# Performance work log

Hardware: AMD Instinct MI355X
Metric: run time of the kernel (lower is better)

Reference implementation:

```python
import jax, jax.numpy as jnp
import numpy as np

B, N = 8, 8192
S_ATTN, S_NONE = 128, 384          # npoint = (npoint_all=512, npoint_none_attn=384) -> npoint_attn=128
S = S_ATTN + S_NONE
NSAMPLE = 64
RADIUS = 0.4
D_FEAT = 64
MLP = [64, 64, 128]
IN_CH = 3 + D_FEAT


def fps(pts, K):
    # pytorch3d.sample_farthest_points, start index 0, full lengths. pts: [B,N,3]
    B_, N_, _ = pts.shape
    def body(carry, _):
        min_d2, last = carry
        lp = jnp.take_along_axis(pts, last[:, None, None], axis=1)      # [B,1,3]
        d2 = jnp.sum((pts - lp) ** 2, -1)                               # [B,N]
        min_d2 = jnp.minimum(min_d2, d2)
        nxt = jnp.argmax(min_d2, -1).astype(jnp.int32)
        return (min_d2, nxt), last
    init = (jnp.full((B_, N_), jnp.float32(1e10)), jnp.zeros((B_,), jnp.int32))
    _, idxs = jax.lax.scan(body, init, None, length=K)
    idxs = idxs.T                                                       # [B,K]
    sampled = jnp.take_along_axis(pts, idxs[..., None], axis=1)         # [B,K,3]
    return sampled, idxs


def ball_query(query, pts, K, radius):
    # pytorch3d.ball_query: first K points with d2 < r^2 in index order; idx pad=-1, nn pad=0.
    d2 = jnp.sum((query[:, :, None, :] - pts[:, None, :, :]) ** 2, -1)  # [B,S,N]
    mask = d2 < radius * radius
    order = jnp.cumsum(mask.astype(jnp.int32), -1) - 1
    slot = jnp.where(mask & (order < K), order, K)                      # overflow -> dump slot K
    n_ids = jnp.broadcast_to(jnp.arange(pts.shape[1], dtype=jnp.int32), slot.shape)
    def scatter_row(slot_row, ids_row):
        return jnp.full((K + 1,), -1, jnp.int32).at[slot_row].set(ids_row)[:K]
    idx = jax.vmap(jax.vmap(scatter_row))(slot, n_ids)                  # [B,S,K]
    valid = idx >= 0
    gathered = jax.vmap(lambda p, i: p[i])(pts, jnp.where(valid, idx, 0))  # [B,S,K,3]
    nn = jnp.where(valid[..., None], gathered, 0.0)
    return idx, nn


def _forward(xyz, points, attention, ws, bs):
    xyz_t = xyz.transpose(0, 2, 1)            # [B,N,3]
    pts_t = points.transpose(0, 2, 1)         # [B,N,D]
    attn_t = attention.transpose(0, 2, 1)     # [B,N,1]

    attn_xyz = attn_t * xyz_t
    none_xyz = (1.0 - attn_t) * xyz_t
    new_attn_xyz, idx_a = fps(attn_xyz, S_ATTN)
    new_none_xyz, idx_n = fps(none_xyz, S_NONE)
    new_xyz = jnp.concatenate([new_attn_xyz, new_none_xyz], axis=1)     # [B,S,3]
    fps_idx = jnp.concatenate([idx_a, idx_n], axis=1)                   # [B,S]
    new_attention = jnp.take_along_axis(attn_t, fps_idx[..., None], axis=1)  # [B,S,1]

    idx, grouped_xyz = ball_query(new_xyz, xyz_t, NSAMPLE, RADIUS)
    grouped_norm = grouped_xyz - new_xyz[:, :, None, :]                 # [B,S,K,3]
    gather_idx = jnp.where(idx < 0, N - 1, idx)   # torch index -1 wraps to last point
    grouped_pts = jax.vmap(lambda p, i: p[i])(pts_t, gather_idx)        # [B,S,K,D]
    feat = jnp.concatenate([grouped_norm, grouped_pts], -1)             # [B,S,K,3+D]

    x = feat.transpose(0, 3, 2, 1)                                      # [B,C,K,S]
    for w, b in zip(ws, bs):                                            # 1x1 Conv2d + ReLU
        x = jax.nn.relu(jnp.einsum('oc,bcks->boks', w, x) + b[None, :, None, None])
    new_points = jnp.max(x, axis=2)                                     # MaxPool over nsample -> [B,C',S]
    return new_xyz.transpose(0, 2, 1), new_points, new_attention.transpose(0, 2, 1)


def setup_inputs() -> dict:
    key = jax.random.key(0)
    ks = jax.random.split(key, 8)
    xyz = jax.random.normal(ks[0], (B, 3, N), jnp.float32)
    points = jax.random.normal(ks[1], (B, D_FEAT, N), jnp.float32)
    attention = jnp.round(jax.random.uniform(ks[2], (B, 1, N), jnp.float32))  # 0/1 mask
    inp = {'xyz': xyz, 'points': points, 'attention': attention}
    last = IN_CH
    for i, oc in enumerate(MLP):
        inp[f'w{i}'] = jax.random.normal(ks[3 + i], (oc, last), jnp.float32) / np.float32(np.sqrt(last))
        inp[f'b{i}'] = jnp.zeros((oc,), jnp.float32)
        last = oc
    return inp


def reference(xyz, points, attention, w0, b0, w1, b1, w2, b2):
    return _forward(xyz, points, attention, (w0, w1, w2), (b0, b1, b2))
```

## Files before the change

### kernel.cpp

```cpp
#include <hip/hip_runtime.h>
#include <cstdint>
#include <cstddef>

#define NB 8
#define NPTS 8192
#define S_TOT 512
#define NSAMP 64
#define DFEAT 64
#define INCH 67
#define SLOTS 17
#define CCAP (SLOTS * 256)
#define TDONE 1060
#define BALLW 13568

typedef __attribute__((ext_vector_type(8))) short v8s;
typedef __attribute__((ext_vector_type(4))) short v4s;
typedef __attribute__((ext_vector_type(4))) float v4f;

__device__ __forceinline__ float d2_exact(float ax, float ay, float az,
                                          float bx, float by, float bz) {
    float dx = __fsub_rn(ax, bx);
    float dy = __fsub_rn(ay, by);
    float dz = __fsub_rn(az, bz);
    return __fadd_rn(__fadd_rn(__fmul_rn(dx, dx), __fmul_rn(dy, dy)), __fmul_rn(dz, dz));
}

__device__ __forceinline__ unsigned short f2b(float f) {
    unsigned u = __float_as_uint(f);
    return (unsigned short)((u + 0x7fffu + ((u >> 16) & 1u)) >> 16);
}

__device__ __forceinline__ void st_wt_f32(float* p, float v) {
    __hip_atomic_store(p, v, __ATOMIC_RELAXED, __HIP_MEMORY_SCOPE_AGENT);
}
__device__ __forceinline__ void st_wt_u32(unsigned* p, unsigned v) {
    __hip_atomic_store(p, v, __ATOMIC_RELAXED, __HIP_MEMORY_SCOPE_AGENT);
}

template <int CTRL>
__device__ __forceinline__ unsigned long long dpp_max_u64(unsigned long long k) {
    int lo = (int)(unsigned)(k & 0xffffffffull);
    int hi = (int)(unsigned)(k >> 32);
    int slo = __builtin_amdgcn_update_dpp(lo, lo, CTRL, 0xf, 0xf, false);
    int shi = __builtin_amdgcn_update_dpp(hi, hi, CTRL, 0xf, 0xf, false);
    unsigned long long o = ((unsigned long long)(unsigned)shi << 32) | (unsigned)slo;
    return (o > k) ? o : k;
}

__device__ __forceinline__ void ball_one(
    const float* __restrict__ xyz,
    const unsigned short* __restrict__ ptsTh,
    const unsigned short* __restrict__ wp,
    const float* __restrict__ b0, const float* __restrict__ b1,
    const float* __restrict__ b2,
    const float* __restrict__ out0, float* __restrict__ out1,
    int b, int sg, int lane, short* sBuf, int* s_idx)
{
    const float R2 = (float)(0.4 * 0.4);
    int col = lane & 15, quad = lane >> 4, kq = quad * 8;

    const float* xb = xyz + (size_t)b * 3 * NPTS;
    float qx = out0[(size_t)b * 3 * S_TOT + sg];
    float qy = out0[(size_t)b * 3 * S_TOT + S_TOT + sg];
    float qz = out0[(size_t)b * 3 * S_TOT + 2 * S_TOT + sg];

    unsigned long long* s_mask = (unsigned long long*)sBuf;

#pragma unroll 8
    for (int j = 0; j < 128; j++) {
        int n = j * 64 + lane;
        float d2 = d2_exact(qx, qy, qz, xb[n], xb[NPTS + n], xb[2 * NPTS + n]);
        unsigned long long m = __ballot(d2 < R2);
        if (lane == 0) s_mask[j] = m;
    }

    unsigned long long m0 = s_mask[lane];
    unsigned long long m1 = s_mask[64 + lane];
    int c0 = (int)__popcll(m0), c1 = (int)__popcll(m1);
    int i0 = c0;
#pragma unroll
    for (int off = 1; off <= 32; off <<= 1) {
        int t = __shfl_up(i0, off);
        if (lane >= off) i0 += t;
    }
    int T0 = __shfl(i0, 63);
    int i1 = c1;
#pragma unroll
    for (int off = 1; off <= 32; off <<= 1) {
        int t = __shfl_up(i1, off);
        if (lane >= off) i1 += t;
    }
    int total = T0 + __shfl(i1, 63);
    int p0 = i0 - c0;
    int p1 = T0 + i1 - c1;

    {
        int base = p0, org = lane * 64;
        while (m0 && base < NSAMP) {
            int bp = __ffsll((long long)m0) - 1;
            s_idx[base++] = org + bp;
            m0 &= m0 - 1;
        }
        base = p1; org = (64 + lane) * 64;
        while (m1 && base < NSAMP) {
            int bp = __ffsll((long long)m1) - 1;
            s_idx[base++] = org + bp;
            m1 &= m1 - 1;
        }
    }
    int cnt = (total > NSAMP) ? NSAMP : total;

    int nb = (lane < cnt) ? s_idx[lane] : -1;
    float nx_ = 0.f, ny_ = 0.f, nz_ = 0.f;
    if (nb >= 0) { nx_ = xb[nb]; ny_ = xb[NPTS + nb]; nz_ = xb[2 * NPTS + nb]; }
    float fx = nx_ - qx, fy = ny_ - qy, fz = nz_ - qz;
    int row = (nb < 0) ? (NPTS - 1) : nb;

    {
        const unsigned short* ph = ptsTh + ((size_t)b * NPTS + row) * DFEAT;
        short* xr = &sBuf[lane * 104];
#pragma unroll
        for (int i = 0; i < 8; i++)
            *(v8s*)(xr + i * 8) = *(const v8s*)(ph + i * 8);
#pragma unroll
        for (int i = 0; i < 5; i++)
            *(v8s*)(xr + 64 + i * 8) = (v8s)0;
        v4s xyzp;
        xyzp[0] = (short)f2b(fx); xyzp[1] = (short)f2b(fy);
        xyzp[2] = (short)f2b(fz); xyzp[3] = 0;
        *(v4s*)(xr + 64) = xyzp;
    }

    const v8s* wpv = (const v8s*)wp;

    v4f acc[4][4];
#pragma unroll
    for (int nt = 0; nt < 4; nt++) {
        float bb = b0[nt * 16 + col];
#pragma unroll
        for (int mt = 0; mt < 4; mt++) acc[mt][nt] = (v4f){bb, bb, bb, bb};
    }
#pragma unroll
    for (int kt = 0; kt < 3; kt++) {
        v8s bf[4];
#pragma unroll
        for (int nt = 0; nt < 4; nt++) bf[nt] = wpv[(kt * 4 + nt) * 64 + lane];
#pragma unroll
        for (int mt = 0; mt < 4; mt++) {
            v8s a = *(const v8s*)&sBuf[(mt * 16 + col) * 104 + kt * 32 + kq];
#pragma unroll
            for (int nt = 0; nt < 4; nt++)
                acc[mt][nt] = __builtin_amdgcn_mfma_f32_16x16x32_bf16(a, bf[nt], acc[mt][nt], 0, 0, 0);
        }
    }
#pragma unroll
    for (int mt = 0; mt < 4; mt++)
#pragma unroll
        for (int nt = 0; nt < 4; nt++)
#pragma unroll
            for (int r = 0; r < 4; r++)
                sBuf[(mt * 16 + quad * 4 + r) * 72 + nt * 16 + col] =
                    (short)f2b(fmaxf(acc[mt][nt][r], 0.0f));

#pragma unroll
    for (int nt = 0; nt < 4; nt++) {
        float bb = b1[nt * 16 + col];
#pragma unroll
        for (int mt = 0; mt < 4; mt++) acc[mt][nt] = (v4f){bb, bb, bb, bb};
    }
#pragma unroll
    for (int kt = 0; kt < 2; kt++) {
        v8s bf[4];
#pragma unroll
        for (int nt = 0; nt < 4; nt++) bf[nt] = wpv[(12 + kt * 4 + nt) * 64 + lane];
#pragma unroll
        for (int mt = 0; mt < 4; mt++) {
            v8s a = *(const v8s*)&sBuf[(mt * 16 + col) * 72 + kt * 32 + kq];
#pragma unroll
            for (int nt = 0; nt < 4; nt++)
                acc[mt][nt] = __builtin_amdgcn_mfma_f32_16x16x32_bf16(a, bf[nt], acc[mt][nt], 0, 0, 0);
        }
    }
#pragma unroll
    for (int mt = 0; mt < 4; mt++)
#pragma unroll
        for (int nt = 0; nt < 4; nt++)
#pragma unroll
            for (int r = 0; r < 4; r++)
                sBuf[(mt * 16 + quad * 4 + r) * 72 + nt * 16 + col] =
                    (short)f2b(fmaxf(acc[mt][nt][r], 0.0f));

#pragma unroll
    for (int p = 0; p < 2; p++) {
#pragma unroll
        for (int nt = 0; nt < 4; nt++) {
            float bb = b2[(p * 4 + nt) * 16 + col];
#pragma unroll
            for (int mt = 0; mt < 4; mt++) acc[mt][nt] = (v4f){bb, bb, bb, bb};
        }
#pragma unroll
        for (int kt = 0; kt < 2; kt++) {
            v8s bf[4];
#pragma unroll
            for (int nt = 0; nt < 4; nt++)
                bf[nt] = wpv[(20 + kt * 8 + p * 4 + nt) * 64 + lane];
#pragma unroll
            for (int mt = 0; mt < 4; mt++) {
                v8s a = *(const v8s*)&sBuf[(mt * 16 + col) * 72 + kt * 32 + kq];
#pragma unroll
                for (int nt = 0; nt < 4; nt++)
                    acc[mt][nt] = __builtin_amdgcn_mfma_f32_16x16x32_bf16(a, bf[nt], acc[mt][nt], 0, 0, 0);
            }
        }
#pragma unroll
        for (int nt = 0; nt < 4; nt++) {
            float v = 0.0f;
#pragma unroll
            for (int mt = 0; mt < 4; mt++)
#pragma unroll
                for (int r = 0; r < 4; r++)
                    v = fmaxf(v, acc[mt][nt][r]);
            v = fmaxf(v, __shfl_xor(v, 16));
            v = fmaxf(v, __shfl_xor(v, 32));
            if (lane < 16)
                out1[((size_t)(b * 128 + (p * 4 + nt) * 16 + lane)) * S_TOT + sg] = v;
        }
    }
}

__global__ __launch_bounds__(256, 1) void fps_fused(
    const float* __restrict__ attn,
    int* __restrict__ hdr,
    float* __restrict__ out0, float* __restrict__ out2,
    const float* __restrict__ pts, unsigned short* __restrict__ ptsTh,
    const float* __restrict__ w0, const float* __restrict__ w1,
    const float* __restrict__ w2, unsigned short* __restrict__ wp,
    const float* __restrict__ xyz,
    const float* __restrict__ b0v, const float* __restrict__ b1v,
    const float* __restrict__ b2v,
    float* __restrict__ out1,
    int* __restrict__ prog, int* __restrict__ tcount, int* __restrict__ skip)
{
    __shared__ __align__(16) char smem[69632 + 6144 + 64];
    int blk = blockIdx.x;
    int tid = threadIdx.x;

    if (blk < 16) {
        int b = blk >> 1, grp = blk & 1;
        int K = grp ? 384 : 128;
        int soff = grp ? 128 : 0;
        int lane = tid & 63, wid = tid >> 6;
        const float* xb = xyz + (size_t)b * 3 * NPTS;
        const float* ab = attn + (size_t)b * NPTS;

        float4* sc = (float4*)smem;
        float4* s_obuf = (float4*)(smem + 69632);
        unsigned long long* s_red = (unsigned long long*)(smem + 69632 + 6144);
        int* s_init = (int*)(smem + 69632 + 6144);

        if (tid == 0) s_init[0] = NPTS;
        __syncthreads();

        int n0 = tid * 32;
        unsigned km = 0;
        int cnt = 0;
#pragma unroll
        for (int c = 0; c < 8; c++) {
            float4 a4 = *(const float4*)(ab + n0 + c * 4);
            const float* af = (const float*)&a4;
#pragma unroll
            for (int j = 0; j < 4; j++) {
                bool kp = grp ? (af[j] == 0.0f) : (af[j] != 0.0f);
                if (kp) { km |= 1u << (c * 4 + j); cnt++; }
            }
        }
        if (km != 0xFFFFFFFFu)
            atomicMin(&s_init[0], n0 + __builtin_ctz(~km));

        int incl = cnt;
#pragma unroll
        for (int off = 1; off <= 32; off <<= 1) {
            int t = __shfl_up(incl, off);
            if (lane >= off) incl += t;
        }
        if (lane == 63) s_init[1 + wid] = incl;
        __syncthreads();
        int woff = 0, tot = 0;
#pragma unroll
        for (int w = 0; w < 4; w++) {
            int v = s_init[1 + w];
            if (w < wid) woff += v;
            tot += v;
        }
        int rm = s_init[0];
        int M = tot + ((rm < NPTS) ? 1 : 0);
        int repslot = (rm < NPTS) ? rm : -1;
        if (tid == 0) { hdr[blk * 2] = M; hdr[blk * 2 + 1] = repslot; }
        if (M > CCAP) {
            if (tid == 0)
                __hip_atomic_store(&prog[blk], -1, __ATOMIC_RELAXED, __HIP_MEMORY_SCOPE_AGENT);
            return;
        }
        int pos = woff + incl - cnt;
        int rm_eff = (rm < NPTS) ? rm : 0x7fffffff;
#pragma unroll
        for (int c = 0; c < 8; c++) {
            if ((km >> (c * 4)) & 0xFu) {
                float4 xx = *(const float4*)(xb + n0 + c * 4);
                float4 yy = *(const float4*)(xb + NPTS + n0 + c * 4);
                float4 zz = *(const float4*)(xb + 2 * NPTS + n0 + c * 4);
                const float* xf = (const float*)&xx;
                const float* yf = (const float*)&yy;
                const float* zf = (const float*)&zz;
#pragma unroll
                for (int j = 0; j < 4; j++) {
                    if ((km >> (c * 4 + j)) & 1u) {
                        int idx = n0 + c * 4 + j;
                        int fin = pos + ((idx > rm_eff) ? 1 : 0);
                        sc[fin] = make_float4(xf[j], yf[j], zf[j], 0.0f);
                        pos++;
                    }
                }
            }
        }
        if (tid == 0 && rm < NPTS)
            sc[rm] = make_float4(__fmul_rn(0.0f, xb[rm]),
                                 __fmul_rn(0.0f, xb[NPTS + rm]),
                                 __fmul_rn(0.0f, xb[2 * NPTS + rm]), 0.0f);
        __syncthreads();
        __builtin_amdgcn_s_setprio(1);

        float px[SLOTS], py[SLOTS], pz[SLOTS], md[SLOTS];
#pragma unroll
        for (int i = 0; i < SLOTS; i++) {
            int sl = i * 256 + tid;
            bool v = sl < M;
            float4 c = sc[sl];
            px[i] = v ? c.x : 0.0f;
            py[i] = v ? c.y : 0.0f;
            pz[i] = v ? c.z : 0.0f;
            md[i] = v ? 1e10f : -1.0f;
        }
        float4 c0 = sc[0];
        float lx = c0.x, ly = c0.y, lz = c0.z;
        float a_last = ab[0];
        float kept_a = grp ? 0.0f : 1.0f;
        float rep_a  = grp ? 1.0f : 0.0f;

        for (int k = 0; k < K; k++) {
            if (tid == 0) s_obuf[k] = make_float4(lx, ly, lz, a_last);
            if (k == K - 1) break;

            float bv = -1.0f; int bslot = 0x7fffffff;
#pragma unroll
            for (int i = 0; i < SLOTS; i++) {
                float d2 = d2_exact(px[i], py[i], pz[i], lx, ly, lz);
                md[i] = fminf(md[i], d2);
                int sl = i * 256 + tid;
                bool w = (md[i] > bv) || ((md[i] == bv) && (sl < bslot));
                bv = w ? md[i] : bv;
                bslot = w ? sl : bslot;
            }
            unsigned long long key = (bv >= 0.0f)
                ? (((unsigned long long)__float_as_uint(bv) << 32) | (unsigned)(~bslot))
                : 0ull;
            key = dpp_max_u64<0x111>(key);
            key = dpp_max_u64<0x112>(key);
            key = dpp_max_u64<0x114>(key);
            key = dpp_max_u64<0x118>(key);
            key = dpp_max_u64<0x142>(key);
            key = dpp_max_u64<0x143>(key);
            int buf = k & 1;
            if (lane == 63) s_red[buf * 4 + wid] = key;
            __syncthreads();

            const unsigned long long* rp = &s_red[buf * 4];
            unsigned long long k0 = rp[0], k1 = rp[1], k2 = rp[2], k3 = rp[3];
            unsigned long long m01 = (k0 > k1) ? k0 : k1;
            unsigned long long m23 = (k2 > k3) ? k2 : k3;
            unsigned long long g = (m01 > m23) ? m01 : m23;
            int wslot = (int)(~(unsigned)g);
            float4 wc = sc[wslot];
            lx = wc.x; ly = wc.y; lz = wc.z;
            a_last = (wslot == repslot) ? rep_a : kept_a;

            if (((k & 15) == 15) && wid == 3) {
                asm volatile("s_waitcnt vmcnt(0)" ::: "memory");
                if (lane == 0 && k >= 31)
                    __hip_atomic_store(&prog[blk], k - 15, __ATOMIC_RELAXED, __HIP_MEMORY_SCOPE_AGENT);
                if (lane < 16) {
                    int kk = k - 15 + lane;
                    float4 o = s_obuf[kk];
                    int sgO = soff + kk;
                    size_t base = (size_t)b * 3 * S_TOT;
                    st_wt_f32(&out0[base + sgO], o.x);
                    st_wt_f32(&out0[base + S_TOT + sgO], o.y);
                    st_wt_f32(&out0[base + 2 * S_TOT + sgO], o.z);
                    st_wt_f32(&out2[(size_t)b * S_TOT + sgO], o.w);
                }
            }
        }
        __syncthreads();
        if (wid == 3) {
            if (lane < 16) {
                int kk = K - 16 + lane;
                float4 o = s_obuf[kk];
                int sgO = soff + kk;
                size_t base = (size_t)b * 3 * S_TOT;
                st_wt_f32(&out0[base + sgO], o.x);
                st_wt_f32(&out0[base + S_TOT + sgO], o.y);
                st_wt_f32(&out0[base + 2 * S_TOT + sgO], o.z);
                st_wt_f32(&out2[(size_t)b * S_TOT + sgO], o.w);
            }
            asm volatile("s_waitcnt vmcnt(0)" ::: "memory");
            if (lane == 0)
                __hip_atomic_store(&prog[blk], K, __ATOMIC_RELAXED, __HIP_MEMORY_SCOPE_AGENT);
        }
    } else if (blk < 16 + 1024) {
        float (*t)[65] = (float(*)[65])smem;
        int blk2 = blk - 16;
        int b = blk2 >> 7;
        int n0 = (blk2 & 127) * 64;
        int tx = tid & 63, ty = tid >> 6;
        for (int c = ty; c < 64; c += 4)
            t[c][tx] = pts[((size_t)b * DFEAT + c) * NPTS + n0 + tx];
        __syncthreads();
        {
            unsigned* pTu = (unsigned*)ptsTh;
            int txc = tid & 31, rr = tid >> 5;
            for (int r = rr; r < 64; r += 8) {
                unsigned lo = f2b(t[2 * txc][r]);
                unsigned hi = f2b(t[2 * txc + 1][r]);
                st_wt_u32(&pTu[((size_t)b * NPTS + n0 + r) * 32 + txc],
                          lo | (hi << 16));
            }
        }
        asm volatile("s_waitcnt vmcnt(0)" ::: "memory");
        __syncthreads();
        if (tid == 0)
            __hip_atomic_fetch_add(tcount, 1, __ATOMIC_RELAXED, __HIP_MEMORY_SCOPE_AGENT);
    } else if (blk < 1076) {
        if (tid < 64) {
            int t = blk - (16 + 1024), l = tid;
            int kq = (l >> 4) * 8, n16 = l & 15;
            unsigned short o[8];
#pragma unroll
            for (int j = 0; j < 8; j++) {
                float v;
                if (t < 12) {
                    int kt = t >> 2, nt = t & 3;
                    int k = kt * 32 + kq + j, n = nt * 16 + n16;
                    v = (k < 64) ? w0[n * INCH + 3 + k] : (k < 67 ? w0[n * INCH + (k - 64)] : 0.0f);
                } else if (t < 20) {
                    int tt = t - 12, kt = tt >> 2, nt = tt & 3;
                    v = w1[(nt * 16 + n16) * 64 + kt * 32 + kq + j];
                } else {
                    int tt = t - 20, kt = tt >> 3, nt = tt & 7;
                    v = w2[(nt * 16 + n16) * 64 + kt * 32 + kq + j];
                }
                o[j] = f2b(v);
            }
            unsigned* wpu = (unsigned*)wp;
            size_t baseu = (size_t)t * 256 + l * 4;
#pragma unroll
            for (int j = 0; j < 4; j++)
                st_wt_u32(&wpu[baseu + j],
                          (unsigned)o[2 * j] | ((unsigned)o[2 * j + 1] << 16));
            asm volatile("s_waitcnt vmcnt(0)" ::: "memory");
            if (tid == 0)
                __hip_atomic_fetch_add(tcount, 1, __ATOMIC_RELAXED, __HIP_MEMORY_SCOPE_AGENT);
        }
    } else {
        int lane = tid & 63, wid = tid >> 6;
        int w = (blk - 1076) * 4 + wid;
        int b, grp, kk;
        if (w < 2048) { kk = w >> 4; int r = w & 15; b = r & 7; grp = r >> 3; }
        else          { int w2 = w - 2048; kk = 128 + (w2 >> 3); b = w2 & 7; grp = 1; }
        int sg = (grp ? 128 : 0) + kk;
        int q = b * 512 + sg;
        int pblk = b * 2 + grp;

        int ok = 1;
        for (int to = 0;;) {
            int p = __hip_atomic_load(&prog[pblk], __ATOMIC_RELAXED, __HIP_MEMORY_SCOPE_AGENT);
            if (p < 0) { ok = 0; break; }
            if (p > kk) {
                int t = __hip_atomic_load(tcount, __ATOMIC_RELAXED, __HIP_MEMORY_SCOPE_AGENT);
                if (t >= TDONE) break;
            }
            if (++to > 500) { ok = 0; break; }
            __builtin_amdgcn_s_sleep(64);
        }
        if (!ok) {
            if (lane == 0) skip[q] = 1;
            return;
        }
        __builtin_amdgcn_fence(__ATOMIC_ACQUIRE, "agent");

        short* sBufW = (short*)(smem + wid * BALLW);
        int* s_idxW = (int*)(smem + wid * BALLW + 13312);
        ball_one(xyz, ptsTh, wp, b0v, b1v, b2v, out0, out1, b, sg, lane, sBufW, s_idxW);
    }
}

__global__ __launch_bounds__(1024, 1) void fps_kernel(
    const float* __restrict__ xyz, const float* __restrict__ attn,
    const int* __restrict__ hdr,
    float* __restrict__ out0, float* __restrict__ out2)
{
    int blk = blockIdx.x;
    if (hdr != nullptr && hdr[blk * 2] <= CCAP) return;
    int b = blk >> 1, grp = blk & 1;
    int K = grp ? 384 : 128;
    int soff = grp ? 128 : 0;
    int tid = threadIdx.x, lane = tid & 63, wid = tid >> 6;
    const float* xb = xyz + (size_t)b * 3 * NPTS;
    const float* ab = attn + (size_t)b * NPTS;

    float px[8], py[8], pz[8], md[8];
#pragma unroll
    for (int i = 0; i < 8; i++) {
        int n = tid + i * 1024;
        float a = ab[n];
        float f = grp ? __fsub_rn(1.0f, a) : a;
        px[i] = __fmul_rn(f, xb[n]);
        py[i] = __fmul_rn(f, xb[NPTS + n]);
        pz[i] = __fmul_rn(f, xb[2 * NPTS + n]);
        md[i] = 1e10f;
    }
    __shared__ unsigned long long s_red[2][16];
    float a_last = ab[0];
    float f0 = grp ? __fsub_rn(1.0f, a_last) : a_last;
    float lx = __fmul_rn(f0, xb[0]);
    float ly = __fmul_rn(f0, xb[NPTS]);
    float lz = __fmul_rn(f0, xb[2 * NPTS]);

    for (int k = 0; k < K; k++) {
        if (tid == 0) {
            int sg = soff + k;
            out0[(size_t)b * 3 * S_TOT + sg] = lx;
            out0[(size_t)b * 3 * S_TOT + S_TOT + sg] = ly;
            out0[(size_t)b * 3 * S_TOT + 2 * S_TOT + sg] = lz;
            out2[(size_t)b * S_TOT + sg] = a_last;
        }
        if (k == K - 1) break;
        float bv = -1.0f; int bi = 0;
#pragma unroll
        for (int i = 0; i < 8; i++) {
            float d2 = d2_exact(px[i], py[i], pz[i], lx, ly, lz);
            md[i] = fminf(md[i], d2);
            if (md[i] > bv) { bv = md[i]; bi = tid + i * 1024; }
        }
        unsigned long long best =
            ((unsigned long long)__float_as_uint(bv) << 32) | (unsigned)(~bi);
#pragma unroll
        for (int off = 32; off >= 1; off >>= 1) {
            unsigned long long o = __shfl_down(best, off);
            best = (o > best) ? o : best;
        }
        if (lane == 0) s_red[k & 1][wid] = best;
        __syncthreads();
        unsigned long long r = (lane < 16) ? s_red[k & 1][lane] : 0ull;
#pragma unroll
        for (int off = 8; off >= 1; off >>= 1) {
            unsigned long long o = __shfl_down(r, off);
            r = (o > r) ? o : r;
        }
        r = __shfl(r, 0);
        int n = (int)(~(unsigned)r);
        a_last = ab[n];
        float fl = grp ? __fsub_rn(1.0f, a_last) : a_last;
        lx = __fmul_rn(fl, xb[n]);
        ly = __fmul_rn(fl, xb[NPTS + n]);
        lz = __fmul_rn(fl, xb[2 * NPTS + n]);
    }
}

__global__ __launch_bounds__(256) void ball_tail(
    const float* __restrict__ xyz,
    const unsigned short* __restrict__ ptsTh,
    const unsigned short* __restrict__ wp,
    const float* __restrict__ b0, const float* __restrict__ b1,
    const float* __restrict__ b2,
    const float* __restrict__ out0, float* __restrict__ out1,
    const int* __restrict__ skip)
{
    __shared__ __align__(16) char smem[4 * BALLW];
    int lane = threadIdx.x & 63, wid = threadIdx.x >> 6;
    int q = blockIdx.x * 4 + wid;
    if (skip[q] == 0) return;
    int b = q >> 9, sg = q & 511;
    short* sBufW = (short*)(smem + wid * BALLW);
    int* s_idxW = (int*)(smem + wid * BALLW + 13312);
    ball_one(xyz, ptsTh, wp, b0, b1, b2, out0, out1, b, sg, lane, sBufW, s_idxW);
}

__global__ __launch_bounds__(64, 1) void ball_mlp_fb(
    const float* __restrict__ xyz, const float* __restrict__ pts,
    const float* __restrict__ w0, const float* __restrict__ b0,
    const float* __restrict__ w1, const float* __restrict__ b1,
    const float* __restrict__ w2, const float* __restrict__ b2,
    const float* __restrict__ out0, float* __restrict__ out1)
{
    const float R2 = (float)(0.4 * 0.4);
    int q = blockIdx.x;
    int b = q >> 9, sg = q & 511, lane = threadIdx.x;
    const float* xb = xyz + (size_t)b * 3 * NPTS;
    float qx = out0[(size_t)b * 3 * S_TOT + sg];
    float qy = out0[(size_t)b * 3 * S_TOT + S_TOT + sg];
    float qz = out0[(size_t)b * 3 * S_TOT + 2 * S_TOT + sg];

    __shared__ int s_idx[NSAMP];
    __shared__ float s_h[32 * 64];
    int cnt = 0;
    for (int base = 0; base < NPTS; base += 64) {
        int n = base + lane;
        float d2 = d2_exact(qx, qy, qz, xb[n], xb[NPTS + n], xb[2 * NPTS + n]);
        bool flag = d2 < R2;
        unsigned long long m = __ballot(flag);
        int pos = cnt + (int)__popcll(m & ((1ull << lane) - 1ull));
        if (flag && pos < NSAMP) s_idx[pos] = n;
        cnt += (int)__popcll(m);
    }
    if (cnt > NSAMP) cnt = NSAMP;
    int nb = (lane < cnt) ? s_idx[lane] : -1;
    float nx_ = 0.f, ny_ = 0.f, nz_ = 0.f;
    if (nb >= 0) { nx_ = xb[nb]; ny_ = xb[NPTS + nb]; nz_ = xb[2 * NPTS + nb]; }
    float fx = nx_ - qx, fy = ny_ - qy, fz = nz_ - qz;
    int row = (nb < 0) ? (NPTS - 1) : nb;

    float h1[64];
#pragma unroll
    for (int o = 0; o < 64; o++) {
        float a = __builtin_fmaf(w0[o * INCH + 0], fx, b0[o]);
        a = __builtin_fmaf(w0[o * INCH + 1], fy, a);
        h1[o] = __builtin_fmaf(w0[o * INCH + 2], fz, a);
    }
    const float* pb = pts + (size_t)b * DFEAT * NPTS + row;
#pragma unroll 1
    for (int c = 0; c < 64; c++) {
        float f = pb[(size_t)c * NPTS];
#pragma unroll
        for (int o = 0; o < 64; o++)
            h1[o] = __builtin_fmaf(w0[o * INCH + 3 + c], f, h1[o]);
    }
#pragma unroll
    for (int c = 0; c < 32; c++) s_h[c * 64 + lane] = fmaxf(h1[c], 0.0f);
    float h1h[32];
#pragma unroll
    for (int c = 0; c < 32; c++) h1h[c] = fmaxf(h1[32 + c], 0.0f);

    float h2[64];
#pragma unroll
    for (int o = 0; o < 64; o++) h2[o] = b1[o];
#pragma unroll 1
    for (int c = 0; c < 32; c++) {
        float hc = s_h[c * 64 + lane];
#pragma unroll
        for (int o = 0; o < 64; o++)
            h2[o] = __builtin_fmaf(w1[o * 64 + c], hc, h2[o]);
    }
#pragma unroll
    for (int c = 0; c < 32; c++) s_h[c * 64 + lane] = h1h[c];
#pragma unroll 1
    for (int c = 0; c < 32; c++) {
        float hc = s_h[c * 64 + lane];
#pragma unroll
        for (int o = 0; o < 64; o++)
            h2[o] = __builtin_fmaf(w1[o * 64 + (32 + c)], hc, h2[o]);
    }
#pragma unroll
    for (int o = 0; o < 64; o++) h2[o] = fmaxf(h2[o], 0.0f);

#pragma unroll 2
    for (int o = 0; o < 128; o++) {
        const float* wr = w2 + o * 64;
        float acc = b2[o];
#pragma unroll
        for (int c = 0; c < 64; c++) acc = __builtin_fmaf(wr[c], h2[c], acc);
        acc = fmaxf(acc, 0.0f);
#pragma unroll
        for (int off = 32; off >= 1; off >>= 1)
            acc = fmaxf(acc, __shfl_down(acc, off));
        if (lane == 0) out1[((size_t)(b * 128 + o)) * S_TOT + sg] = acc;
    }
}

extern "C" void kernel_launch(void* const* d_in, const int* in_sizes, int n_in,
                              void* d_out, int out_size, void* d_ws, size_t ws_size,
                              hipStream_t stream) {
    const float* xyz  = (const float*)d_in[0];
    const float* pts  = (const float*)d_in[1];
    const float* attn = (const float*)d_in[2];
    const float* w0 = (const float*)d_in[3];
    const float* b0 = (const float*)d_in[4];
    const float* w1 = (const float*)d_in[5];
    const float* b1 = (const float*)d_in[6];
    const float* w2 = (const float*)d_in[7];
    const float* b2 = (const float*)d_in[8];

    float* out0 = (float*)d_out;
    float* out1 = out0 + (size_t)NB * 3 * S_TOT;
    float* out2 = out1 + (size_t)NB * 128 * S_TOT;

    unsigned short* wp    = (unsigned short*)d_ws;
    unsigned short* ptsTh = (unsigned short*)((char*)d_ws + 36864);
    char*           cxyz  = (char*)d_ws + 36864 + 8388608;
    int*            hdr   = (int*)(cxyz + (size_t)16 * CCAP * 16);
    int*            prog  = hdr + 32;
    int*            tcnt  = prog + 16;
    int*            skip  = tcnt + 4;
    const size_t need = 36864 + 8388608 + (size_t)16 * CCAP * 16 + 128
                        + (16 + 4 + 4096) * 4 + 64;

    if (ws_size >= need) {
        hipMemsetAsync(prog, 0, (size_t)(16 + 4 + 4096) * 4, stream);
        fps_fused<<<16 + 1024 + 36 + 1024, 256, 0, stream>>>(
            attn, hdr, out0, out2, pts, ptsTh, w0, w1, w2, wp,
            xyz, b0, b1, b2, out1, prog, tcnt, skip);
        fps_kernel<<<16, 1024, 0, stream>>>(xyz, attn, hdr, out0, out2);
        ball_tail<<<1024, 256, 0, stream>>>(xyz, ptsTh, wp, b0, b1, b2,
                                            out0, out1, skip);
    } else {
        fps_kernel<<<16, 1024, 0, stream>>>(xyz, attn, nullptr, out0, out2);
        ball_mlp_fb<<<NB * S_TOT, 64, 0, stream>>>(xyz, pts, w0, b0, w1, b1,
                                                   w2, b2, out0, out1);
    }
}
```

Measured before the change: 611.5 us.

## Split FPS compaction into producer blocks and merge fallback and tail into one cleanup kernel

Point compaction moves out of the 16 FPS blocks into 16 separate producer blocks. These write the compacted coordinates to global workspace and raise a flag, and the FPS blocks spin on that flag before loading into registers and shared memory. The FPS inner-loop barrier becomes a raw s_waitcnt plus s_barrier, and an extra progress value is published earlier. The separate fps_kernel and ball_tail launches are replaced by one cleanup kernel that reruns FPS only for blocks that failed or overflowed, then handles the skipped ball queries once a counter is set. This cuts one launch and shortens the FPS critical path, but it adds cross-block spin-waits with timeouts that assume producer blocks get scheduled alongside the waiting blocks.

```diff
diff --git a/kernel.cpp b/kernel.cpp
--- a/kernel.cpp
+++ b/kernel.cpp
@@ -12,6 +12,7 @@
 #define CCAP (SLOTS * 256)
 #define TDONE 1060
 #define BALLW 13568
+#define SMEMSZ 82048
 
 typedef __attribute__((ext_vector_type(8))) short v8s;
 typedef __attribute__((ext_vector_type(4))) short v4s;
@@ -230,6 +231,7 @@
 
 __global__ __launch_bounds__(256, 1) void fps_fused(
     const float* __restrict__ attn,
+    float4* __restrict__ cxyz,
     int* __restrict__ hdr,
     float* __restrict__ out0, float* __restrict__ out2,
     const float* __restrict__ pts, unsigned short* __restrict__ ptsTh,
@@ -239,9 +241,10 @@
     const float* __restrict__ b0v, const float* __restrict__ b1v,
     const float* __restrict__ b2v,
     float* __restrict__ out1,
-    int* __restrict__ prog, int* __restrict__ tcount, int* __restrict__ skip)
+    int* __restrict__ prog, int* __restrict__ tcount, int* __restrict__ skip,
+    int* __restrict__ cflag, int* __restrict__ fpsdone)
 {
-    __shared__ __align__(16) char smem[69632 + 6144 + 64];
+    __shared__ __align__(16) char smem[SMEMSZ];
     int blk = blockIdx.x;
     int tid = threadIdx.x;
 
@@ -250,102 +253,49 @@
         int K = grp ? 384 : 128;
         int soff = grp ? 128 : 0;
         int lane = tid & 63, wid = tid >> 6;
-        const float* xb = xyz + (size_t)b * 3 * NPTS;
-        const float* ab = attn + (size_t)b * NPTS;
-
-        float4* sc = (float4*)smem;
-        float4* s_obuf = (float4*)(smem + 69632);
-        unsigned long long* s_red = (unsigned long long*)(smem + 69632 + 6144);
-        int* s_init = (int*)(smem + 69632 + 6144);
-
-        if (tid == 0) s_init[0] = NPTS;
-        __syncthreads();
-
-        int n0 = tid * 32;
-        unsigned km = 0;
-        int cnt = 0;
-#pragma unroll
-        for (int c = 0; c < 8; c++) {
-            float4 a4 = *(const float4*)(ab + n0 + c * 4);
-            const float* af = (const float*)&a4;
-#pragma unroll
-            for (int j = 0; j < 4; j++) {
-                bool kp = grp ? (af[j] == 0.0f) : (af[j] != 0.0f);
-                if (kp) { km |= 1u << (c * 4 + j); cnt++; }
-            }
-        }
-        if (km != 0xFFFFFFFFu)
-            atomicMin(&s_init[0], n0 + __builtin_ctz(~km));
-
-        int incl = cnt;
-#pragma unroll
-        for (int off = 1; off <= 32; off <<= 1) {
-            int t = __shfl_up(incl, off);
-            if (lane >= off) incl += t;
-        }
-        if (lane == 63) s_init[1 + wid] = incl;
-        __syncthreads();
-        int woff = 0, tot = 0;
-#pragma unroll
-        for (int w = 0; w < 4; w++) {
-            int v = s_init[1 + w];
-            if (w < wid) woff += v;
-            tot += v;
-        }
-        int rm = s_init[0];
-        int M = tot + ((rm < NPTS) ? 1 : 0);
-        int repslot = (rm < NPTS) ? rm : -1;
-        if (tid == 0) { hdr[blk * 2] = M; hdr[blk * 2 + 1] = repslot; }
+
+        int cok = 0;
+        for (int to = 0; to < 4000; ++to) {
+            if (__hip_atomic_load(&cflag[blk], __ATOMIC_RELAXED, __HIP_MEMORY_SCOPE_AGENT)) { cok = 1; break; }
+            __builtin_amdgcn_s_sleep(32);
+        }
+        if (!cok) {
+            if (tid == 0)
+                __hip_atomic_store(&prog[blk], -1, __ATOMIC_RELAXED, __HIP_MEMORY_SCOPE_AGENT);
+            return;
+        }
+        __builtin_amdgcn_fence(__ATOMIC_ACQUIRE, "agent");
+
+        int M = hdr[blk * 2];
+        int repslot = hdr[blk * 2 + 1];
         if (M > CCAP) {
             if (tid == 0)
                 __hip_atomic_store(&prog[blk], -1, __ATOMIC_RELAXED, __HIP_MEMORY_SCOPE_AGENT);
             return;
         }
-        int pos = woff + incl - cnt;
-        int rm_eff = (rm < NPTS) ? rm : 0x7fffffff;
-#pragma unroll
-        for (int c = 0; c < 8; c++) {
-            if ((km >> (c * 4)) & 0xFu) {
-                float4 xx = *(const float4*)(xb + n0 + c * 4);
-                float4 yy = *(const float4*)(xb + NPTS + n0 + c * 4);
-                float4 zz = *(const float4*)(xb + 2 * NPTS + n0 + c * 4);
-                const float* xf = (const float*)&xx;
-                const float* yf = (const float*)&yy;
-                const float* zf = (const float*)&zz;
-#pragma unroll
-                for (int j = 0; j < 4; j++) {
-                    if ((km >> (c * 4 + j)) & 1u) {
-                        int idx = n0 + c * 4 + j;
-                        int fin = pos + ((idx > rm_eff) ? 1 : 0);
-                        sc[fin] = make_float4(xf[j], yf[j], zf[j], 0.0f);
-                        pos++;
-                    }
-                }
-            }
-        }
-        if (tid == 0 && rm < NPTS)
-            sc[rm] = make_float4(__fmul_rn(0.0f, xb[rm]),
-                                 __fmul_rn(0.0f, xb[NPTS + rm]),
-                                 __fmul_rn(0.0f, xb[2 * NPTS + rm]), 0.0f);
-        __syncthreads();
         __builtin_amdgcn_s_setprio(1);
+
+        const float4* cb = cxyz + (size_t)blk * CCAP;
+        float4* sc = (float4*)smem;
+        float4* s_obuf = (float4*)(smem + 69632);
+        unsigned long long* s_red = (unsigned long long*)(smem + 69632 + 6144);
 
         float px[SLOTS], py[SLOTS], pz[SLOTS], md[SLOTS];
 #pragma unroll
         for (int i = 0; i < SLOTS; i++) {
             int sl = i * 256 + tid;
             bool v = sl < M;
-            float4 c = sc[sl];
-            px[i] = v ? c.x : 0.0f;
-            py[i] = v ? c.y : 0.0f;
-            pz[i] = v ? c.z : 0.0f;
+            float4 c = v ? cb[sl] : make_float4(0.f, 0.f, 0.f, 0.f);
+            px[i] = c.x; py[i] = c.y; pz[i] = c.z;
+            sc[sl] = c;
             md[i] = v ? 1e10f : -1.0f;
         }
-        float4 c0 = sc[0];
+        float4 c0 = cb[0];
         float lx = c0.x, ly = c0.y, lz = c0.z;
-        float a_last = ab[0];
+        float a_last = attn[(size_t)b * NPTS];
         float kept_a = grp ? 0.0f : 1.0f;
         float rep_a  = grp ? 1.0f : 0.0f;
+        __syncthreads();
 
         for (int k = 0; k < K; k++) {
             if (tid == 0) s_obuf[k] = make_float4(lx, ly, lz, a_last);
@@ -372,7 +322,8 @@
             key = dpp_max_u64<0x143>(key);
             int buf = k & 1;
             if (lane == 63) s_red[buf * 4 + wid] = key;
-            __syncthreads();
+            asm volatile("s_waitcnt lgkmcnt(0)\n\ts_barrier" ::: "memory");
+            __builtin_amdgcn_sched_barrier(0);
 
             const unsigned long long* rp = &s_red[buf * 4];
             unsigned long long k0 = rp[0], k1 = rp[1], k2 = rp[2], k3 = rp[3];
@@ -402,6 +353,8 @@
         }
         __syncthreads();
         if (wid == 3) {
+            if (lane == 0)
+                __hip_atomic_store(&prog[blk], K - 16, __ATOMIC_RELAXED, __HIP_MEMORY_SCOPE_AGENT);
             if (lane < 16) {
                 int kk = K - 16 + lane;
                 float4 o = s_obuf[kk];
@@ -413,12 +366,100 @@
                 st_wt_f32(&out2[(size_t)b * S_TOT + sgO], o.w);
             }
             asm volatile("s_waitcnt vmcnt(0)" ::: "memory");
-            if (lane == 0)
+            if (lane == 0) {
                 __hip_atomic_store(&prog[blk], K, __ATOMIC_RELAXED, __HIP_MEMORY_SCOPE_AGENT);
-        }
-    } else if (blk < 16 + 1024) {
+                st_wt_u32((unsigned*)&fpsdone[blk], 1u);
+            }
+        }
+    } else if (blk < 32) {
+        int cblk = blk - 16;
+        int b = cblk >> 1, grp = cblk & 1;
+        int lane = tid & 63, wid = tid >> 6;
+        const float* xb = xyz + (size_t)b * 3 * NPTS;
+        const float* ab = attn + (size_t)b * NPTS;
+        float* c4f = (float*)(cxyz + (size_t)cblk * CCAP);
+
+        int* s_init = (int*)smem;
+        if (tid == 0) s_init[0] = NPTS;
+        __syncthreads();
+
+        int n0 = tid * 32;
+        unsigned km = 0;
+        int cnt = 0;
+#pragma unroll
+        for (int c = 0; c < 8; c++) {
+            float4 a4 = *(const float4*)(ab + n0 + c * 4);
+            const float* af = (const float*)&a4;
+#pragma unroll
+            for (int j = 0; j < 4; j++) {
+                bool kp = grp ? (af[j] == 0.0f) : (af[j] != 0.0f);
+                if (kp) { km |= 1u << (c * 4 + j); cnt++; }
+            }
+        }
+        if (km != 0xFFFFFFFFu)
+            atomicMin(&s_init[0], n0 + __builtin_ctz(~km));
+
+        int incl = cnt;
+#pragma unroll
+        for (int off = 1; off <= 32; off <<= 1) {
+            int t = __shfl_up(incl, off);
+            if (lane >= off) incl += t;
+        }
+        if (lane == 63) s_init[1 + wid] = incl;
+        __syncthreads();
+        int woff = 0, tot = 0;
+#pragma unroll
+        for (int w = 0; w < 4; w++) {
+            int v = s_init[1 + w];
+            if (w < wid) woff += v;
+            tot += v;
+        }
+        int rm = s_init[0];
+        int M = tot + ((rm < NPTS) ? 1 : 0);
+        if (tid == 0) {
+            st_wt_u32((unsigned*)&hdr[cblk * 2], (unsigned)M);
+            st_wt_u32((unsigned*)&hdr[cblk * 2 + 1], (unsigned)((rm < NPTS) ? rm : -1));
+        }
+        if (M <= CCAP) {
+            int pos = woff + incl - cnt;
+            int rm_eff = (rm < NPTS) ? rm : 0x7fffffff;
+#pragma unroll
+            for (int c = 0; c < 8; c++) {
+                if ((km >> (c * 4)) & 0xFu) {
+                    float4 xx = *(const float4*)(xb + n0 + c * 4);
+                    float4 yy = *(const float4*)(xb + NPTS + n0 + c * 4);
+                    float4 zz = *(const float4*)(xb + 2 * NPTS + n0 + c * 4);
+                    const float* xf = (const float*)&xx;
+                    const float* yf = (const float*)&yy;
+                    const float* zf = (const float*)&zz;
+#pragma unroll
+                    for (int j = 0; j < 4; j++) {
+                        if ((km >> (c * 4 + j)) & 1u) {
+                            int idx = n0 + c * 4 + j;
+                            int fin = pos + ((idx > rm_eff) ? 1 : 0);
+                            st_wt_f32(c4f + (size_t)fin * 4 + 0, xf[j]);
+                            st_wt_f32(c4f + (size_t)fin * 4 + 1, yf[j]);
+                            st_wt_f32(c4f + (size_t)fin * 4 + 2, zf[j]);
+                            st_wt_f32(c4f + (size_t)fin * 4 + 3, 0.0f);
+                            pos++;
+                        }
+                    }
+                }
+            }
+            if (tid == 0 && rm < NPTS) {
+                st_wt_f32(c4f + (size_t)rm * 4 + 0, __fmul_rn(0.0f, xb[rm]));
+                st_wt_f32(c4f + (size_t)rm * 4 + 1, __fmul_rn(0.0f, xb[NPTS + rm]));
+                st_wt_f32(c4f + (size_t)rm * 4 + 2, __fmul_rn(0.0f, xb[2 * NPTS + rm]));
+                st_wt_f32(c4f + (size_t)rm * 4 + 3, 0.0f);
+            }
+        }
+        asm volatile("s_waitcnt vmcnt(0)" ::: "memory");
+        __syncthreads();
+        if (tid == 0)
+            __hip_atomic_store(&cflag[cblk], 1, __ATOMIC_RELAXED, __HIP_MEMORY_SCOPE_AGENT);
+    } else if (blk < 32 + 1024) {
         float (*t)[65] = (float(*)[65])smem;
-        int blk2 = blk - 16;
+        int blk2 = blk - 32;
         int b = blk2 >> 7;
         int n0 = (blk2 & 127) * 64;
         int tx = tid & 63, ty = tid >> 6;
@@ -439,9 +480,9 @@
         __syncthreads();
         if (tid == 0)
             __hip_atomic_fetch_add(tcount, 1, __ATOMIC_RELAXED, __HIP_MEMORY_SCOPE_AGENT);
-    } else if (blk < 1076) {
+    } else if (blk < 1092) {
         if (tid < 64) {
-            int t = blk - (16 + 1024), l = tid;
+            int t = blk - (32 + 1024), l = tid;
             int kq = (l >> 4) * 8, n16 = l & 15;
             unsigned short o[8];
 #pragma unroll
@@ -472,7 +513,7 @@
         }
     } else {
         int lane = tid & 63, wid = tid >> 6;
-        int w = (blk - 1076) * 4 + wid;
+        int w = (blk - 1092) * 4 + wid;
         int b, grp, kk;
         if (w < 2048) { kk = w >> 4; int r = w & 15; b = r & 7; grp = r >> 3; }
         else          { int w2 = w - 2048; kk = 128 + (w2 >> 3); b = w2 & 7; grp = 1; }
@@ -500,6 +541,123 @@
         short* sBufW = (short*)(smem + wid * BALLW);
         int* s_idxW = (int*)(smem + wid * BALLW + 13312);
         ball_one(xyz, ptsTh, wp, b0v, b1v, b2v, out0, out1, b, sg, lane, sBufW, s_idxW);
+    }
+}
+
+__global__ __launch_bounds__(1024, 1) void cleanup(
+    const float* __restrict__ xyz, const float* __restrict__ attn,
+    const int* __restrict__ hdr,
+    float* __restrict__ out0, float* __restrict__ out2,
+    const unsigned short* __restrict__ ptsTh,
+    const unsigned short* __restrict__ wp,
+    const float* __restrict__ b0, const float* __restrict__ b1,
+    const float* __restrict__ b2,
+    float* __restrict__ out1,
+    const int* __restrict__ skip,
+    const int* __restrict__ fpsdone, int* __restrict__ fpsfb)
+{
+    __shared__ __align__(16) char smem[4 * BALLW];
+    int blk = blockIdx.x;
+    int tid = threadIdx.x;
+
+    if (blk < 16) {
+        int need = (fpsdone[blk] == 0) || (hdr[blk * 2] > CCAP);
+        if (!need) {
+            if (tid == 0)
+                __hip_atomic_fetch_add(fpsfb, 1, __ATOMIC_RELAXED, __HIP_MEMORY_SCOPE_AGENT);
+            return;
+        }
+        unsigned long long* s_red = (unsigned long long*)smem;
+        int b = blk >> 1, grp = blk & 1;
+        int K = grp ? 384 : 128;
+        int soff = grp ? 128 : 0;
+        int lane = tid & 63, wid = tid >> 6;
+        const float* xb = xyz + (size_t)b * 3 * NPTS;
+        const float* ab = attn + (size_t)b * NPTS;
+
+        float px[8], py[8], pz[8], md[8];
+#pragma unroll
+        for (int i = 0; i < 8; i++) {
+            int n = tid + i * 1024;
+            float a = ab[n];
+            float f = grp ? __fsub_rn(1.0f, a) : a;
+            px[i] = __fmul_rn(f, xb[n]);
+            py[i] = __fmul_rn(f, xb[NPTS + n]);
+            pz[i] = __fmul_rn(f, xb[2 * NPTS + n]);
+            md[i] = 1e10f;
+        }
+        float a_last = ab[0];
+        float f0 = grp ? __fsub_rn(1.0f, a_last) : a_last;
+        float lx = __fmul_rn(f0, xb[0]);
+        float ly = __fmul_rn(f0, xb[NPTS]);
+        float lz = __fmul_rn(f0, xb[2 * NPTS]);
+
+        for (int k = 0; k < K; k++) {
+            if (tid == 0) {
+                int sg = soff + k;
+                out0[(size_t)b * 3 * S_TOT + sg] = lx;
+                out0[(size_t)b * 3 * S_TOT + S_TOT + sg] = ly;
+                out0[(size_t)b * 3 * S_TOT + 2 * S_TOT + sg] = lz;
+                out2[(size_t)b * S_TOT + sg] = a_last;
+            }
+            if (k == K - 1) break;
+            float bv = -1.0f; int bi = 0;
+#pragma unroll
+            for (int i = 0; i < 8; i++) {
+                float d2 = d2_exact(px[i], py[i], pz[i], lx, ly, lz);
+                md[i] = fminf(md[i], d2);
+                if (md[i] > bv) { bv = md[i]; bi = tid + i * 1024; }
+            }
+            unsigned long long best =
+                ((unsigned long long)__float_as_uint(bv) << 32) | (unsigned)(~bi);
+#pragma unroll
+            for (int off = 32; off >= 1; off >>= 1) {
+                unsigned long long o = __shfl_down(best, off);
+                best = (o > best) ? o : best;
+            }
+            if (lane == 0) s_red[(k & 1) * 16 + wid] = best;
+            __syncthreads();
+            unsigned long long r = (lane < 16) ? s_red[(k & 1) * 16 + lane] : 0ull;
+#pragma unroll
+            for (int off = 8; off >= 1; off >>= 1) {
+                unsigned long long o = __shfl_down(r, off);
+                r = (o > r) ? o : r;
+            }
+            r = __shfl(r, 0);
+            int n = (int)(~(unsigned)r);
+            a_last = ab[n];
+            float fl = grp ? __fsub_rn(1.0f, a_last) : a_last;
+            lx = __fmul_rn(fl, xb[n]);
+            ly = __fmul_rn(fl, xb[NPTS + n]);
+            lz = __fmul_rn(fl, xb[2 * NPTS + n]);
+        }
+        __syncthreads();
+        if (tid == 0) {
+            __builtin_amdgcn_fence(__ATOMIC_RELEASE, "agent");
+            __hip_atomic_fetch_add(fpsfb, 1, __ATOMIC_RELAXED, __HIP_MEMORY_SCOPE_AGENT);
+        }
+    } else {
+        if (tid >= 256) return;
+        int lane = tid & 63, wid = tid >> 6;
+        int q0 = ((blk - 16) * 4 + wid) * 16;
+        int any = 0;
+#pragma unroll 1
+        for (int i = 0; i < 16; i++) any |= skip[q0 + i];
+        if (!any) return;
+        for (int to = 0; to < 4000; ++to) {
+            if (__hip_atomic_load(fpsfb, __ATOMIC_RELAXED, __HIP_MEMORY_SCOPE_AGENT) >= 16) break;
+            __builtin_amdgcn_s_sleep(64);
+        }
+        __builtin_amdgcn_fence(__ATOMIC_ACQUIRE, "agent");
+        short* sBufW = (short*)(smem + wid * BALLW);
+        int* s_idxW = (int*)(smem + wid * BALLW + 13312);
+#pragma unroll 1
+        for (int i = 0; i < 16; i++) {
+            int q = q0 + i;
+            if (skip[q] == 0) continue;
+            int b = q >> 9, sg = q & 511;
+            ball_one(xyz, ptsTh, wp, b0, b1, b2, out0, out1, b, sg, lane, sBufW, s_idxW);
+        }
     }
 }
 
@@ -574,25 +732,6 @@
         ly = __fmul_rn(fl, xb[NPTS + n]);
         lz = __fmul_rn(fl, xb[2 * NPTS + n]);
     }
-}
-
-__global__ __launch_bounds__(256) void ball_tail(
-    const float* __restrict__ xyz,
-    const unsigned short* __restrict__ ptsTh,
-    const unsigned short* __restrict__ wp,
-    const float* __restrict__ b0, const float* __restrict__ b1,
-    const float* __restrict__ b2,
-    const float* __restrict__ out0, float* __restrict__ out1,
-    const int* __restrict__ skip)
-{
-    __shared__ __align__(16) char smem[4 * BALLW];
-    int lane = threadIdx.x & 63, wid = threadIdx.x >> 6;
-    int q = blockIdx.x * 4 + wid;
-    if (skip[q] == 0) return;
-    int b = q >> 9, sg = q & 511;
-    short* sBufW = (short*)(smem + wid * BALLW);
-    int* s_idxW = (int*)(smem + wid * BALLW + 13312);
-    ball_one(xyz, ptsTh, wp, b0, b1, b2, out0, out1, b, sg, lane, sBufW, s_idxW);
 }
 
 __global__ __launch_bounds__(64, 1) void ball_mlp_fb(
@@ -705,22 +844,25 @@
 
     unsigned short* wp    = (unsigned short*)d_ws;
     unsigned short* ptsTh = (unsigned short*)((char*)d_ws + 36864);
-    char*           cxyz  = (char*)d_ws + 36864 + 8388608;
-    int*            hdr   = (int*)(cxyz + (size_t)16 * CCAP * 16);
+    float4*         cxyz  = (float4*)((char*)d_ws + 36864 + 8388608);
+    int*            hdr   = (int*)((char*)cxyz + (size_t)16 * CCAP * 16);
     int*            prog  = hdr + 32;
     int*            tcnt  = prog + 16;
     int*            skip  = tcnt + 4;
+    int*            cflag = skip + 4096;
+    int*            fpsdn = cflag + 16;
+    int*            fpsfb = fpsdn + 16;
+    const size_t ctrl_bytes = (size_t)(16 + 4 + 4096 + 16 + 16 + 16) * 4;
     const size_t need = 36864 + 8388608 + (size_t)16 * CCAP * 16 + 128
-                        + (16 + 4 + 4096) * 4 + 64;
+                        + ctrl_bytes + 64;
 
     if (ws_size >= need) {
-        hipMemsetAsync(prog, 0, (size_t)(16 + 4 + 4096) * 4, stream);
-        fps_fused<<<16 + 1024 + 36 + 1024, 256, 0, stream>>>(
-            attn, hdr, out0, out2, pts, ptsTh, w0, w1, w2, wp,
-            xyz, b0, b1, b2, out1, prog, tcnt, skip);
-        fps_kernel<<<16, 1024, 0, stream>>>(xyz, attn, hdr, out0, out2);
-        ball_tail<<<1024, 256, 0, stream>>>(xyz, ptsTh, wp, b0, b1, b2,
-                                            out0, out1, skip);
+        hipMemsetAsync(prog, 0, ctrl_bytes, stream);
+        fps_fused<<<16 + 16 + 1024 + 36 + 1024, 256, 0, stream>>>(
+            attn, cxyz, hdr, out0, out2, pts, ptsTh, w0, w1, w2, wp,
+            xyz, b0, b1, b2, out1, prog, tcnt, skip, cflag, fpsdn);
+        cleanup<<<80, 1024, 0, stream>>>(xyz, attn, hdr, out0, out2, ptsTh, wp,
+                                         b0, b1, b2, out1, skip, fpsdn, fpsfb);
     } else {
         fps_kernel<<<16, 1024, 0, stream>>>(xyz, attn, nullptr, out0, out2);
         ball_mlp_fb<<<NB * S_TOT, 64, 0, stream>>>(xyz, pts, w0, b0, w1, b1,
```

New measurement: 611.7 us. No clear change (+0.0%).
